# Kernel tuning notes

Hardware: AMD Instinct MI355X
Metric: run time of the kernel (lower is better)

Reference implementation:

```python
import jax, jax.numpy as jnp
import numpy as np

B, S, T = 32, 128, 64
V, E, H = 32000, 256, 512


def setup_inputs() -> dict:
    key = jax.random.key(0)
    ks = jax.random.split(key, 32)
    n = jax.random.normal

    def lin(k, fi, fo):
        kw, kb = jax.random.split(k)
        s = 1.0 / np.sqrt(fi)
        return (jax.random.uniform(kw, (fi, fo), jnp.float32, -s, s),
                jax.random.uniform(kb, (fo,), jnp.float32, -s, s))

    W_enc, b_enc = lin(ks[4], 2 * H, H)      # attention.enc_h_in
    W_prev, b_prev = lin(ks[5], H, H)        # attention.prev_s_in
    W_att, b_att = lin(ks[6], H, 1)          # attention.linear
    Wi_g, bi_g = lin(ks[7], E, 2 * H)        # cell.input_weights
    Wh_g, bh_g = lin(ks[8], H, 2 * H)        # cell.hidden_weights
    Wc_g, bc_g = lin(ks[9], 2 * H, 2 * H)    # cell.ctx_weights
    Wi, bi = lin(ks[10], E, H)               # cell.input_in
    Wh, bh = lin(ks[11], H, H)               # cell.hidden_in
    Wc, bc = lin(ks[12], 2 * H, H)           # cell.ctx_in
    W_out, b_out = lin(ks[13], H, V)         # dec2word

    return dict(
        content=n(ks[0], (B, H), jnp.float32),
        sentiment=n(ks[1], (B, H), jnp.float32),
        hiddens=n(ks[2], (B, S, 2 * H), jnp.float32),
        target=jax.random.randint(ks[3], (B, T), 0, V, jnp.int32),
        embed=n(ks[14], (V, E), jnp.float32) * 0.02,
        W_enc=W_enc, b_enc=b_enc, W_prev=W_prev, b_prev=b_prev,
        W_att=W_att, b_att=b_att,
        Wi_g=Wi_g, bi_g=bi_g, Wh_g=Wh_g, bh_g=bh_g, Wc_g=Wc_g, bc_g=bc_g,
        Wi=Wi, bi=bi, Wh=Wh, bh=bh, Wc=Wc, bc=bc,
        W_out=W_out, b_out=b_out,
    )


def reference(content, sentiment, hiddens, target, embed,
              W_enc, b_enc, W_prev, b_prev, W_att, b_att,
              Wi_g, bi_g, Wh_g, bh_g, Wc_g, bc_g,
              Wi, bi, Wh, bh, Wc, bc, W_out, b_out):
    tgt_emb = embed[target]                       # [B, T, E]
    enc_proj = hiddens @ W_enc + b_enc            # [B, S, H], timestep-invariant

    def step(prev_s, x_t):
        # additive attention
        q = prev_s @ W_prev + b_prev              # [B, H]
        h = jnp.tanh(enc_proj + q[:, None, :])    # [B, S, H]
        score = h @ W_att + b_att                 # [B, S, 1]
        alpha = jax.nn.softmax(score, axis=1)     # over source positions
        ctx = jnp.einsum('bsi,bsh->bh', alpha, hiddens)  # [B, 2H]
        # GRU-like cell (original uses only the first gate, as written)
        gates = x_t @ Wi_g + bi_g + prev_s @ Wh_g + bh_g + ctx @ Wc_g + bc_g
        reset_gate, _update_gate = jnp.split(gates, 2, axis=1)
        r = jax.nn.sigmoid(reset_gate)
        s_tilde = jnp.tanh(x_t @ Wi + bi + prev_s @ Wh + bh + ctx @ Wc + bc)
        new_s = (1.0 - r) * prev_s + r * s_tilde
        return new_s, new_s

    _, dec_h = jax.lax.scan(step, content, jnp.swapaxes(tgt_emb, 0, 1))
    dec_h = jnp.swapaxes(dec_h, 0, 1)             # [B, T, H]
    style_logits = sentiment @ W_out + b_out      # [B, V], same every step
    outputs = (dec_h @ W_out + b_out) + 0.5 * style_logits[:, None, :]
    return outputs                                # [B, T, V]
```

## Files before the change

### kernel.cpp

```cpp
#include <hip/hip_runtime.h>
#include <hip/hip_bf16.h>
#include <math.h>

#define NB 32
#define NS 128
#define NT 64
#define NV 32000
#define NE 256
#define NH 512

typedef short s16x8 __attribute__((ext_vector_type(8)));
typedef float f32x4 __attribute__((ext_vector_type(4)));

__device__ __forceinline__ unsigned short f2bf(float x) {
    union { float f; unsigned u; } v; v.f = x;
    unsigned r = v.u + 0x7FFFu + ((v.u >> 16) & 1u);
    return (unsigned short)(r >> 16);
}
__device__ __forceinline__ float bf2f(short h) {
    union { unsigned u; float f; } x;
    x.u = ((unsigned)(unsigned short)h) << 16;
    return x.f;
}

__device__ __forceinline__ void bar_lgkm() {
    asm volatile("s_waitcnt lgkmcnt(0)" ::: "memory");
    __builtin_amdgcn_sched_barrier(0);
    __builtin_amdgcn_s_barrier();
    __builtin_amdgcn_sched_barrier(0);
}

__device__ __forceinline__ void st_pt(unsigned long long* p, unsigned pay, unsigned tag) {
    unsigned long long v = (unsigned long long)pay | ((unsigned long long)tag << 32);
    asm volatile("global_store_dwordx2 %0, %1, off sc0 sc1" :: "v"(p), "v"(v) : "memory");
}
__device__ __forceinline__ void ld8_pt(const unsigned long long* b0, unsigned long long* v) {
    unsigned long long v0, v1, v2, v3, v4, v5, v6, v7;
    asm volatile(
        "global_load_dwordx2 %0, %8, off sc0 sc1\n\t"
        "global_load_dwordx2 %1, %9, off sc0 sc1\n\t"
        "global_load_dwordx2 %2, %10, off sc0 sc1\n\t"
        "global_load_dwordx2 %3, %11, off sc0 sc1\n\t"
        "global_load_dwordx2 %4, %12, off sc0 sc1\n\t"
        "global_load_dwordx2 %5, %13, off sc0 sc1\n\t"
        "global_load_dwordx2 %6, %14, off sc0 sc1\n\t"
        "global_load_dwordx2 %7, %15, off sc0 sc1\n\t"
        "s_waitcnt vmcnt(0)"
        : "=&v"(v0), "=&v"(v1), "=&v"(v2), "=&v"(v3),
          "=&v"(v4), "=&v"(v5), "=&v"(v6), "=&v"(v7)
        : "v"(b0), "v"(b0 + 1024), "v"(b0 + 2048), "v"(b0 + 3072),
          "v"(b0 + 4096), "v"(b0 + 5120), "v"(b0 + 6144), "v"(b0 + 7168)
        : "memory");
    v[0] = v0; v[1] = v1; v[2] = v2; v[3] = v3;
    v[4] = v4; v[5] = v5; v[6] = v6; v[7] = v7;
}
__device__ __forceinline__ void ld3_pt(const unsigned long long* p0,
                                       const unsigned long long* p1,
                                       const unsigned long long* p2,
                                       unsigned long long& a, unsigned long long& b,
                                       unsigned long long& c) {
    asm volatile(
        "global_load_dwordx2 %0, %3, off sc0 sc1\n\t"
        "global_load_dwordx2 %1, %4, off sc0 sc1\n\t"
        "global_load_dwordx2 %2, %5, off sc0 sc1\n\t"
        "s_waitcnt vmcnt(0)"
        : "=&v"(a), "=&v"(b), "=&v"(c)
        : "v"(p0), "v"(p1), "v"(p2)
        : "memory");
}

__global__ void build_wfrag_k(const float* __restrict__ Wp,
                              const float* __restrict__ Whg,
                              const float* __restrict__ Wh,
                              unsigned short* __restrict__ wfrag) {
    int blk = blockIdx.x;
    int lane = threadIdx.x;
    int ct = blk >> 4, kt = blk & 15;
    int c = ct * 16 + (lane & 15);
    int kb = kt * 32 + (lane >> 4) * 8;
    s16x8 v;
#pragma unroll
    for (int j = 0; j < 8; ++j) {
        int k = kb + j;
        float x;
        if (c < 512)       x = Wp[k * 512 + c];
        else if (c < 1024) x = Whg[k * 1024 + (c - 512)];
        else               x = Wh[k * 512 + (c - 1024)];
        v[j] = (short)f2bf(x);
    }
    ((s16x8*)wfrag)[blk * 64 + lane] = v;
}

template<int MODE>
__global__ __launch_bounds__(256, 2) void gemm_mfma(
    const float* __restrict__ Af, const unsigned short* __restrict__ Abf,
    const int* __restrict__ gidx,
    const float* __restrict__ B0, const float* __restrict__ B1, const float* __restrict__ B2,
    const float* __restrict__ e0, const float* __restrict__ e1, const float* __restrict__ e2,
    const float* __restrict__ e3, const float* __restrict__ e4, const float* __restrict__ e5,
    void* __restrict__ O0v, void* __restrict__ O1v, void* __restrict__ O2v)
{
    constexpr int M   = (MODE == 0) ? 4096 : 2048;
    constexpr int K   = (MODE == 0) ? 1024 : ((MODE == 1) ? 256 : 512);
    constexpr int LDA = (MODE == 0) ? 1024 : ((MODE == 1) ? 256 : 512);
    constexpr int MB  = M / 128;

    const int bm = blockIdx.x % MB, bn = blockIdx.x / MB;
    const int m0 = bm * 128, n0 = bn * 128;

    const float* Bp; int ldb, coff;
    if constexpr (MODE == 0) {
        int sub = n0 >> 9;
        Bp   = (sub == 0) ? B0 : (sub == 1) ? B1 : B2;
        ldb  = (sub == 1) ? 1024 : 512;
        coff = n0 & 511;
    } else if constexpr (MODE == 1) {
        if (n0 < 512) { Bp = B0; ldb = 1024; coff = n0; }
        else          { Bp = B1; ldb = 512;  coff = n0 - 512; }
    } else {
        Bp = B0; ldb = 32000; coff = n0;
    }

    __shared__ unsigned short As[128 * 40];
    __shared__ unsigned short Bs[128 * 40];

    const int tid = threadIdx.x, lane = tid & 63, w = tid >> 6;
    const int wr = w >> 1, wc = w & 1;
    const int k0f = (lane >> 4) * 8;
    const int rsel = lane & 15;

    f32x4 acc[4][4];
#pragma unroll
    for (int i = 0; i < 4; ++i)
#pragma unroll
        for (int j = 0; j < 4; ++j) { f32x4 z = {0.f, 0.f, 0.f, 0.f}; acc[i][j] = z; }

    for (int kt = 0; kt < K / 32; ++kt) {
        const int k0 = kt * 32;
        __syncthreads();
#pragma unroll
        for (int i = 0; i < 16; ++i) {
            int idx = tid + i * 256;
            int r = idx >> 5, k = idx & 31;
            unsigned short v;
            if constexpr (MODE == 2) {
                v = Abf[(size_t)(m0 + r) * LDA + k0 + k];
            } else if constexpr (MODE == 1) {
                int g = gidx[m0 + r];
                v = f2bf(Af[(size_t)g * 256 + k0 + k]);
            } else {
                v = f2bf(Af[(size_t)(m0 + r) * LDA + k0 + k]);
            }
            As[r * 40 + k] = v;
        }
#pragma unroll
        for (int i = 0; i < 16; ++i) {
            int idx = tid + i * 256;
            int k = idx >> 7, c = idx & 127;
            Bs[c * 40 + k] = f2bf(Bp[(size_t)(k0 + k) * ldb + coff + c]);
        }
        __syncthreads();

        s16x8 af[4], bf[4];
#pragma unroll
        for (int i = 0; i < 4; ++i)
            af[i] = *(const s16x8*)&As[(wr * 64 + i * 16 + rsel) * 40 + k0f];
#pragma unroll
        for (int j = 0; j < 4; ++j)
            bf[j] = *(const s16x8*)&Bs[(wc * 64 + j * 16 + rsel) * 40 + k0f];
#pragma unroll
        for (int i = 0; i < 4; ++i)
#pragma unroll
            for (int j = 0; j < 4; ++j)
                acc[i][j] = __builtin_amdgcn_mfma_f32_16x16x32_bf16(af[i], bf[j], acc[i][j], 0, 0, 0);
    }

    const int rg = (lane >> 4) * 4;
#pragma unroll
    for (int i = 0; i < 4; ++i)
#pragma unroll
        for (int j = 0; j < 4; ++j) {
            int row0 = m0 + wr * 64 + i * 16 + rg;
            int col  = n0 + wc * 64 + j * 16 + rsel;
            if constexpr (MODE == 0) {
                int sub = col >> 9;
                if (sub == 0) {
                    unsigned short* Ta = (unsigned short*)O0v;
#pragma unroll
                    for (int r = 0; r < 4; ++r)
                        Ta[(size_t)(row0 + r) * 512 + col] = f2bf(tanhf(acc[i][j][r] + e0[col]));
                } else {
                    int h = col & 511;
                    int bb = row0 >> 7, s0 = row0 & 127;
                    unsigned long long pk = 0;
#pragma unroll
                    for (int r = 0; r < 4; ++r)
                        pk |= (unsigned long long)f2bf(acc[i][j][r]) << (16 * r);
                    unsigned short* dstp = (sub == 1) ? (unsigned short*)O1v : (unsigned short*)O2v;
                    *(unsigned long long*)&dstp[(size_t)((bb * 512 + h) * 128 + s0)] = pk;
                }
            } else if constexpr (MODE == 1) {
                float* Of = (float*)O0v;
                float bias;
                if (col < 512) bias = e0[col] + e1[col] + e2[col];
                else { int h = col - 512; bias = e3[h] + e4[h] + e5[h]; }
#pragma unroll
                for (int r = 0; r < 4; ++r)
                    Of[(size_t)(row0 + r) * 1024 + col] = acc[i][j][r] + bias;
            } else {
                float* Of = (float*)O0v;
#pragma unroll
                for (int r = 0; r < 4; ++r)
                    Of[(size_t)(row0 + r) * 32000 + col] = acc[i][j][r] + 1.5f * e0[col];
            }
        }
}

__global__ __launch_bounds__(1024) void scan_df(
    const float* __restrict__ content, const float* __restrict__ sentiment,
    const float* __restrict__ b_prev,  const float* __restrict__ W_att,
    const unsigned short* __restrict__ Ta_bf,
    const unsigned short* __restrict__ hWcg_t,
    const unsigned short* __restrict__ hWc_t,
    const float* __restrict__ xgxs, const unsigned short* __restrict__ wfrag,
    unsigned long long* __restrict__ Spl, unsigned long long* __restrict__ Upl,
    unsigned short* __restrict__ dh)
{
    const int b = blockIdx.x;
    const int tid = threadIdx.x, lane = tid & 63, w = tid >> 6;

    __shared__ unsigned short W_lds[3 * 16 * 64 * 8];
    __shared__ unsigned short S_lds[32 * 536];
    __shared__ float tq[512];
    __shared__ float sc[128], al[128];
    __shared__ float cg[512], cs[512];

    {
        const s16x8* src = (const s16x8*)wfrag + (size_t)b * (3 * 16 * 64);
        s16x8* dst = (s16x8*)W_lds;
        for (int i = tid; i < 3 * 16 * 64; i += 1024) dst[i] = src[i];
    }
    float s_reg = 0.f, senth = 0.f, bprev_h = 0.f;
    if (tid < 512) {
        s_reg   = content[b * 512 + tid];
        senth   = 0.5f * sentiment[b * 512 + tid];
        bprev_h = b_prev[tid];
    }
    float wv[8];
    {
        const f32x4* wa = (const f32x4*)&W_att[lane * 8];
        f32x4 a0 = wa[0], a1 = wa[1];
#pragma unroll
        for (int j = 0; j < 4; ++j) { wv[j] = a0[j]; wv[4 + j] = a1[j]; }
    }
    const int kbase = (lane >> 4) * 8;
    const int mat = tid >> 9, hh = tid & 511;
    const s16x8* Mp = (const s16x8*)((mat ? hWc_t : hWcg_t) + ((size_t)(b * 512 + hh)) * 128);

    if (tid < 512) {
        float nsn = __shfl_down(s_reg, 1, 64);
        if (!(lane & 1)) {
            unsigned pay = (unsigned)f2bf(s_reg) | ((unsigned)f2bf(nsn) << 16);
            st_pt(&Spl[b * 256 + (tid >> 1)], pay, 1u);
        }
    }

    for (int t = 0; t < 64; ++t) {
        const unsigned want = (unsigned)(t + 1);
        const size_t xrow = (size_t)b * 64 + t;
        float xg_pre = 0.f, xs_pre = 0.f;
        if (tid < 512) {
            xg_pre = xgxs[xrow * 1024 + tid];
            xs_pre = xgxs[xrow * 1024 + 512 + tid];
        }

        {
            unsigned long long v[8];
            const unsigned long long* base = &Spl[tid];
            ld8_pt(base, v);
            for (;;) {
                bool ok = true;
#pragma unroll
                for (int ii = 0; ii < 8; ++ii) ok &= ((unsigned)(v[ii] >> 32) == want);
                if (ok) break;
                __builtin_amdgcn_s_sleep(1);
                ld8_pt(base, v);
            }
#pragma unroll
            for (int ii = 0; ii < 8; ++ii) {
                int idx = tid + ii * 1024;
                int r = idx >> 8, c = (idx & 255) * 2;
                *(unsigned*)&S_lds[r * 536 + c] = (unsigned)v[ii];
            }
        }
        bar_lgkm();

        if (w < 6) {
            const int mt = w & 1, ct = w >> 1;
            const int arow = mt * 16 + (lane & 15);
            f32x4 ae = {0.f, 0.f, 0.f, 0.f}, ao = {0.f, 0.f, 0.f, 0.f};
            const s16x8* wl = (const s16x8*)W_lds;
#pragma unroll
            for (int kt = 0; kt < 16; kt += 2) {
                s16x8 a0 = *(const s16x8*)&S_lds[arow * 536 + kt * 32 + kbase];
                s16x8 a1 = *(const s16x8*)&S_lds[arow * 536 + (kt + 1) * 32 + kbase];
                ae = __builtin_amdgcn_mfma_f32_16x16x32_bf16(a0, wl[(ct * 16 + kt) * 64 + lane], ae, 0, 0, 0);
                ao = __builtin_amdgcn_mfma_f32_16x16x32_bf16(a1, wl[(ct * 16 + kt + 1) * 64 + lane], ao, 0, 0, 0);
            }
            f32x4 a4 = ae + ao;
            const int cout = b * 48 + ct * 16 + (lane & 15);
            const int rbase = mt * 16 + (lane >> 4) * 4;
#pragma unroll
            for (int r = 0; r < 4; ++r)
                st_pt(&Upl[(size_t)(rbase + r) * 1536 + cout], __float_as_uint(a4[r]), want);
        }

        float guv = 0.f, suv = 0.f;
        if (tid < 512) {
            unsigned long long u0, u1, u2;
            const unsigned long long* q0 = &Upl[b * 1536 + tid];
            const unsigned long long* q1 = &Upl[b * 1536 + 512 + tid];
            const unsigned long long* q2 = &Upl[b * 1536 + 1024 + tid];
            ld3_pt(q0, q1, q2, u0, u1, u2);
            while (((unsigned)(u0 >> 32) != want) | ((unsigned)(u1 >> 32) != want) |
                   ((unsigned)(u2 >> 32) != want)) {
                __builtin_amdgcn_s_sleep(1);
                ld3_pt(q0, q1, q2, u0, u1, u2);
            }
            float qv = __uint_as_float((unsigned)u0);
            guv = __uint_as_float((unsigned)u1);
            suv = __uint_as_float((unsigned)u2);
            tq[tid] = tanhf(qv + bprev_h);
        }
        bar_lgkm();

        {
            float tqv[8];
            const f32x4* tp = (const f32x4*)&tq[lane * 8];
            f32x4 t0 = tp[0], t1 = tp[1];
#pragma unroll
            for (int j = 0; j < 4; ++j) { tqv[j] = t0[j]; tqv[4 + j] = t1[j]; }
#pragma unroll
            for (int s8 = 0; s8 < 8; ++s8) {
                int s = w * 8 + s8;
                s16x8 tv = *(const s16x8*)&Ta_bf[((size_t)(b * 128 + s)) * 512 + lane * 8];
                float a = 0.f;
#pragma unroll
                for (int j = 0; j < 8; ++j) {
                    float ta = bf2f(tv[j]);
                    float num = ta + tqv[j];
                    float den = fmaf(ta, tqv[j], 1.0f);
                    a = fmaf(wv[j], num * __builtin_amdgcn_rcpf(den), a);
                }
#pragma unroll
                for (int off = 32; off; off >>= 1) a += __shfl_xor(a, off, 64);
                if (lane == 0) sc[s] = a;
            }
        }

        s16x8 hw[8];
#pragma unroll
        for (int q = 0; q < 8; ++q) hw[q] = Mp[q];

        bar_lgkm();
        if (w == 0) {
            float v0 = sc[lane], v1 = sc[lane + 64];
            float m = fmaxf(v0, v1);
#pragma unroll
            for (int off = 32; off; off >>= 1) m = fmaxf(m, __shfl_xor(m, off, 64));
            float p0 = __expf(v0 - m), p1 = __expf(v1 - m);
            float sm = p0 + p1;
#pragma unroll
            for (int off = 32; off; off >>= 1) sm += __shfl_xor(sm, off, 64);
            float inv = __builtin_amdgcn_rcpf(sm);
            al[lane] = p0 * inv; al[lane + 64] = p1 * inv;
        }
        bar_lgkm();

        {
            float a0 = 0.f, a1 = 0.f;
#pragma unroll
            for (int q = 0; q < 8; ++q) {
                s16x8 v = hw[q];
#pragma unroll
                for (int j = 0; j < 8; j += 2) {
                    a0 = fmaf(al[q * 8 + j],     bf2f(v[j]),     a0);
                    a1 = fmaf(al[q * 8 + j + 1], bf2f(v[j + 1]), a1);
                }
            }
#pragma unroll
            for (int q = 8; q < 16; ++q) {
                s16x8 v = Mp[q];
#pragma unroll
                for (int j = 0; j < 8; j += 2) {
                    a0 = fmaf(al[q * 8 + j],     bf2f(v[j]),     a0);
                    a1 = fmaf(al[q * 8 + j + 1], bf2f(v[j + 1]), a1);
                }
            }
            if (mat) cs[hh] = a0 + a1; else cg[hh] = a0 + a1;
        }
        bar_lgkm();

        if (tid < 512) {
            int h = tid;
            float g  = guv + xg_pre + cg[h];
            float r  = __builtin_amdgcn_rcpf(1.0f + __expf(-g));
            float sp = suv + xs_pre + cs[h];
            float e  = __expf(2.0f * sp);
            float st = 1.0f - 2.0f * __builtin_amdgcn_rcpf(e + 1.0f);
            float ns = s_reg + r * (st - s_reg);
            s_reg = ns;
            dh[xrow * 512 + h] = f2bf(ns + senth);
            if (t < 63) {
                float nsn = __shfl_down(ns, 1, 64);
                if (!(lane & 1)) {
                    unsigned pay = (unsigned)f2bf(ns) | ((unsigned)f2bf(nsn) << 16);
                    st_pt(&Spl[b * 256 + (h >> 1)], pay, (unsigned)(t + 2));
                }
            }
        }
        bar_lgkm();
    }
}

extern "C" void kernel_launch(void* const* d_in, const int* in_sizes, int n_in,
                              void* d_out, int out_size, void* d_ws, size_t ws_size,
                              hipStream_t stream) {
    const float* content  = (const float*)d_in[0];
    const float* sentiment= (const float*)d_in[1];
    const float* hiddens  = (const float*)d_in[2];
    const int*   target   = (const int*)  d_in[3];
    const float* embed    = (const float*)d_in[4];
    const float* W_enc = (const float*)d_in[5];  const float* b_enc = (const float*)d_in[6];
    const float* W_prev= (const float*)d_in[7];  const float* b_prev= (const float*)d_in[8];
    const float* W_att = (const float*)d_in[9];
    const float* Wi_g  = (const float*)d_in[11]; const float* bi_g  = (const float*)d_in[12];
    const float* Wh_g  = (const float*)d_in[13]; const float* bh_g  = (const float*)d_in[14];
    const float* Wc_g  = (const float*)d_in[15]; const float* bc_g  = (const float*)d_in[16];
    const float* Wi    = (const float*)d_in[17]; const float* bi    = (const float*)d_in[18];
    const float* Wh    = (const float*)d_in[19]; const float* bh    = (const float*)d_in[20];
    const float* Wc    = (const float*)d_in[21]; const float* bc    = (const float*)d_in[22];
    const float* W_out = (const float*)d_in[23]; const float* b_out = (const float*)d_in[24];
    float* out = (float*)d_out;

    char* ws = (char*)d_ws;
    unsigned short* wfrag = (unsigned short*)ws;
    unsigned long long* Spl = (unsigned long long*)(ws + 0x180000);
    unsigned long long* Upl = (unsigned long long*)(ws + 0x190000);
    unsigned short* Ta_bf   = (unsigned short*)(ws + 0x200000);
    unsigned short* hWcg_t  = (unsigned short*)(ws + 0x600000);
    unsigned short* hWc_t   = (unsigned short*)(ws + 0xA00000);
    float* xgxs     = (float*)(ws + 0xE00000);
    unsigned short* dh      = (unsigned short*)(ws + 0x1600000);

    hipMemsetAsync(ws + 0x180000, 0, 0x70000, stream);

    build_wfrag_k<<<96 * 16, 64, 0, stream>>>(W_prev, Wh_g, Wh, wfrag);

    gemm_mfma<0><<<32 * 12, 256, 0, stream>>>(
        hiddens, nullptr, nullptr, W_enc, Wc_g, Wc,
        b_enc, nullptr, nullptr, nullptr, nullptr, nullptr,
        (void*)Ta_bf, (void*)hWcg_t, (void*)hWc_t);

    gemm_mfma<1><<<16 * 8, 256, 0, stream>>>(
        embed, nullptr, target, Wi_g, Wi, nullptr,
        bi_g, bh_g, bc_g, bi, bh, bc,
        (void*)xgxs, nullptr, nullptr);

    scan_df<<<NB, 1024, 0, stream>>>(
        content, sentiment, b_prev, W_att, Ta_bf, hWcg_t, hWc_t,
        xgxs, wfrag, Spl, Upl, dh);

    gemm_mfma<2><<<16 * 250, 256, 0, stream>>>(
        nullptr, dh, nullptr, W_out, nullptr, nullptr,
        b_out, nullptr, nullptr, nullptr, nullptr, nullptr,
        (void*)out, nullptr, nullptr);

    (void)in_sizes; (void)n_in; (void)out_size; (void)ws_size;
}
```

Baseline: 1.359 ms.

## Fuse output projection into scan kernel, overlapping vocab GEMM with recurrence

Merges the sequential scan and the vocabulary projection GEMM into one persistent launch. Thirty-two blocks run the recurrence and publish per-batch progress counters every 8 timesteps. The remaining 224 blocks spin on those counters and compute 256x256 output tiles for finished timestep groups, so the large GEMM overlaps the latency-bound scan. In exchange the output GEMM now loads its tiles through coherent, uncached loads and converts W_out to bf16 on the fly. The extra co-resident blocks may also compete with the scan blocks for compute units, and the design relies on all blocks being resident at once to avoid deadlock.

```diff
diff --git a/kernel.cpp b/kernel.cpp
--- a/kernel.cpp
+++ b/kernel.cpp
@@ -11,6 +11,7 @@
 
 typedef short s16x8 __attribute__((ext_vector_type(8)));
 typedef float f32x4 __attribute__((ext_vector_type(4)));
+typedef unsigned u32x4 __attribute__((ext_vector_type(4)));
 
 __device__ __forceinline__ unsigned short f2bf(float x) {
     union { float f; unsigned u; } v; v.f = x;
@@ -33,6 +34,21 @@
 __device__ __forceinline__ void st_pt(unsigned long long* p, unsigned pay, unsigned tag) {
     unsigned long long v = (unsigned long long)pay | ((unsigned long long)tag << 32);
     asm volatile("global_store_dwordx2 %0, %1, off sc0 sc1" :: "v"(p), "v"(v) : "memory");
+}
+__device__ __forceinline__ void st_coh32(unsigned* p, unsigned v) {
+    asm volatile("global_store_dword %0, %1, off sc0 sc1" :: "v"(p), "v"(v) : "memory");
+}
+__device__ __forceinline__ unsigned ld_coh32(const unsigned* p) {
+    unsigned v;
+    asm volatile("global_load_dword %0, %1, off sc0 sc1\n\ts_waitcnt vmcnt(0)"
+                 : "=v"(v) : "v"(p) : "memory");
+    return v;
+}
+__device__ __forceinline__ u32x4 ld_coh_x4(const void* p) {
+    u32x4 v;
+    asm volatile("global_load_dwordx4 %0, %1, off sc0 sc1\n\ts_waitcnt vmcnt(0)"
+                 : "=&v"(v) : "v"(p) : "memory");
+    return v;
 }
 __device__ __forceinline__ void ld8_pt(const unsigned long long* b0, unsigned long long* v) {
     unsigned long long v0, v1, v2, v3, v4, v5, v6, v7;
@@ -101,8 +117,8 @@
     void* __restrict__ O0v, void* __restrict__ O1v, void* __restrict__ O2v)
 {
     constexpr int M   = (MODE == 0) ? 4096 : 2048;
-    constexpr int K   = (MODE == 0) ? 1024 : ((MODE == 1) ? 256 : 512);
-    constexpr int LDA = (MODE == 0) ? 1024 : ((MODE == 1) ? 256 : 512);
+    constexpr int K   = (MODE == 0) ? 1024 : 256;
+    constexpr int LDA = (MODE == 0) ? 1024 : 256;
     constexpr int MB  = M / 128;
 
     const int bm = blockIdx.x % MB, bn = blockIdx.x / MB;
@@ -114,11 +130,9 @@
         Bp   = (sub == 0) ? B0 : (sub == 1) ? B1 : B2;
         ldb  = (sub == 1) ? 1024 : 512;
         coff = n0 & 511;
-    } else if constexpr (MODE == 1) {
+    } else {
         if (n0 < 512) { Bp = B0; ldb = 1024; coff = n0; }
         else          { Bp = B1; ldb = 512;  coff = n0 - 512; }
-    } else {
-        Bp = B0; ldb = 32000; coff = n0;
     }
 
     __shared__ unsigned short As[128 * 40];
@@ -143,9 +157,7 @@
             int idx = tid + i * 256;
             int r = idx >> 5, k = idx & 31;
             unsigned short v;
-            if constexpr (MODE == 2) {
-                v = Abf[(size_t)(m0 + r) * LDA + k0 + k];
-            } else if constexpr (MODE == 1) {
+            if constexpr (MODE == 1) {
                 int g = gidx[m0 + r];
                 v = f2bf(Af[(size_t)g * 256 + k0 + k]);
             } else {
@@ -199,7 +211,7 @@
                     unsigned short* dstp = (sub == 1) ? (unsigned short*)O1v : (unsigned short*)O2v;
                     *(unsigned long long*)&dstp[(size_t)((bb * 512 + h) * 128 + s0)] = pk;
                 }
-            } else if constexpr (MODE == 1) {
+            } else {
                 float* Of = (float*)O0v;
                 float bias;
                 if (col < 512) bias = e0[col] + e1[col] + e2[col];
@@ -207,16 +219,11 @@
 #pragma unroll
                 for (int r = 0; r < 4; ++r)
                     Of[(size_t)(row0 + r) * 1024 + col] = acc[i][j][r] + bias;
-            } else {
-                float* Of = (float*)O0v;
-#pragma unroll
-                for (int r = 0; r < 4; ++r)
-                    Of[(size_t)(row0 + r) * 32000 + col] = acc[i][j][r] + 1.5f * e0[col];
-            }
-        }
-}
-
-__global__ __launch_bounds__(1024) void scan_df(
+            }
+        }
+}
+
+__global__ __launch_bounds__(1024) void fused_scan_out(
     const float* __restrict__ content, const float* __restrict__ sentiment,
     const float* __restrict__ b_prev,  const float* __restrict__ W_att,
     const unsigned short* __restrict__ Ta_bf,
@@ -224,202 +231,274 @@
     const unsigned short* __restrict__ hWc_t,
     const float* __restrict__ xgxs, const unsigned short* __restrict__ wfrag,
     unsigned long long* __restrict__ Spl, unsigned long long* __restrict__ Upl,
-    unsigned short* __restrict__ dh)
+    unsigned short* __restrict__ dh, unsigned* __restrict__ prog,
+    const float* __restrict__ W_out, const float* __restrict__ b_out,
+    float* __restrict__ out)
 {
-    const int b = blockIdx.x;
+    __shared__ __attribute__((aligned(16))) char smem[90624];
     const int tid = threadIdx.x, lane = tid & 63, w = tid >> 6;
 
-    __shared__ unsigned short W_lds[3 * 16 * 64 * 8];
-    __shared__ unsigned short S_lds[32 * 536];
-    __shared__ float tq[512];
-    __shared__ float sc[128], al[128];
-    __shared__ float cg[512], cs[512];
-
-    {
-        const s16x8* src = (const s16x8*)wfrag + (size_t)b * (3 * 16 * 64);
-        s16x8* dst = (s16x8*)W_lds;
-        for (int i = tid; i < 3 * 16 * 64; i += 1024) dst[i] = src[i];
-    }
-    float s_reg = 0.f, senth = 0.f, bprev_h = 0.f;
-    if (tid < 512) {
-        s_reg   = content[b * 512 + tid];
-        senth   = 0.5f * sentiment[b * 512 + tid];
-        bprev_h = b_prev[tid];
-    }
-    float wv[8];
-    {
-        const f32x4* wa = (const f32x4*)&W_att[lane * 8];
-        f32x4 a0 = wa[0], a1 = wa[1];
-#pragma unroll
-        for (int j = 0; j < 4; ++j) { wv[j] = a0[j]; wv[4 + j] = a1[j]; }
-    }
-    const int kbase = (lane >> 4) * 8;
-    const int mat = tid >> 9, hh = tid & 511;
-    const s16x8* Mp = (const s16x8*)((mat ? hWc_t : hWcg_t) + ((size_t)(b * 512 + hh)) * 128);
-
-    if (tid < 512) {
-        float nsn = __shfl_down(s_reg, 1, 64);
-        if (!(lane & 1)) {
-            unsigned pay = (unsigned)f2bf(s_reg) | ((unsigned)f2bf(nsn) << 16);
-            st_pt(&Spl[b * 256 + (tid >> 1)], pay, 1u);
-        }
-    }
-
-    for (int t = 0; t < 64; ++t) {
-        const unsigned want = (unsigned)(t + 1);
-        const size_t xrow = (size_t)b * 64 + t;
-        float xg_pre = 0.f, xs_pre = 0.f;
+    if (blockIdx.x < NB) {
+        const int b = blockIdx.x;
+        unsigned short* W_lds = (unsigned short*)smem;
+        unsigned short* S_lds = (unsigned short*)(smem + 49152);
+        float* tq = (float*)(smem + 83456);
+        float* sc = (float*)(smem + 85504);
+        float* al = (float*)(smem + 86016);
+        float* cg = (float*)(smem + 86528);
+        float* cs = (float*)(smem + 88576);
+
+        {
+            const s16x8* src = (const s16x8*)wfrag + (size_t)b * (3 * 16 * 64);
+            s16x8* dst = (s16x8*)W_lds;
+            for (int i = tid; i < 3 * 16 * 64; i += 1024) dst[i] = src[i];
+        }
+        float s_reg = 0.f, senth = 0.f, bprev_h = 0.f;
         if (tid < 512) {
-            xg_pre = xgxs[xrow * 1024 + tid];
-            xs_pre = xgxs[xrow * 1024 + 512 + tid];
-        }
-
+            s_reg   = content[b * 512 + tid];
+            senth   = 0.5f * sentiment[b * 512 + tid];
+            bprev_h = b_prev[tid];
+        }
+        float wv[8];
         {
-            unsigned long long v[8];
-            const unsigned long long* base = &Spl[tid];
-            ld8_pt(base, v);
-            for (;;) {
-                bool ok = true;
-#pragma unroll
-                for (int ii = 0; ii < 8; ++ii) ok &= ((unsigned)(v[ii] >> 32) == want);
-                if (ok) break;
-                __builtin_amdgcn_s_sleep(1);
+            const f32x4* wa = (const f32x4*)&W_att[lane * 8];
+            f32x4 a0 = wa[0], a1 = wa[1];
+#pragma unroll
+            for (int j = 0; j < 4; ++j) { wv[j] = a0[j]; wv[4 + j] = a1[j]; }
+        }
+        const int kbase = (lane >> 4) * 8;
+        const int mat = tid >> 9, hh = tid & 511;
+        const s16x8* Mp = (const s16x8*)((mat ? hWc_t : hWcg_t) + ((size_t)(b * 512 + hh)) * 128);
+
+        if (tid < 512) {
+            float nsn = __shfl_down(s_reg, 1, 64);
+            if (!(lane & 1)) {
+                unsigned pay = (unsigned)f2bf(s_reg) | ((unsigned)f2bf(nsn) << 16);
+                st_pt(&Spl[b * 256 + (tid >> 1)], pay, 1u);
+            }
+        }
+
+        for (int t = 0; t < 64; ++t) {
+            const unsigned want = (unsigned)(t + 1);
+            float xg_pre = 0.f, xs_pre = 0.f;
+            if (tid < 512) {
+                xg_pre = xgxs[((size_t)b * 64 + t) * 1024 + tid];
+                xs_pre = xgxs[((size_t)b * 64 + t) * 1024 + 512 + tid];
+            }
+
+            {
+                unsigned long long v[8];
+                const unsigned long long* base = &Spl[tid];
                 ld8_pt(base, v);
-            }
-#pragma unroll
-            for (int ii = 0; ii < 8; ++ii) {
-                int idx = tid + ii * 1024;
-                int r = idx >> 8, c = (idx & 255) * 2;
-                *(unsigned*)&S_lds[r * 536 + c] = (unsigned)v[ii];
-            }
-        }
-        bar_lgkm();
-
-        if (w < 6) {
-            const int mt = w & 1, ct = w >> 1;
-            const int arow = mt * 16 + (lane & 15);
-            f32x4 ae = {0.f, 0.f, 0.f, 0.f}, ao = {0.f, 0.f, 0.f, 0.f};
-            const s16x8* wl = (const s16x8*)W_lds;
-#pragma unroll
-            for (int kt = 0; kt < 16; kt += 2) {
-                s16x8 a0 = *(const s16x8*)&S_lds[arow * 536 + kt * 32 + kbase];
-                s16x8 a1 = *(const s16x8*)&S_lds[arow * 536 + (kt + 1) * 32 + kbase];
-                ae = __builtin_amdgcn_mfma_f32_16x16x32_bf16(a0, wl[(ct * 16 + kt) * 64 + lane], ae, 0, 0, 0);
-                ao = __builtin_amdgcn_mfma_f32_16x16x32_bf16(a1, wl[(ct * 16 + kt + 1) * 64 + lane], ao, 0, 0, 0);
-            }
-            f32x4 a4 = ae + ao;
-            const int cout = b * 48 + ct * 16 + (lane & 15);
-            const int rbase = mt * 16 + (lane >> 4) * 4;
-#pragma unroll
-            for (int r = 0; r < 4; ++r)
-                st_pt(&Upl[(size_t)(rbase + r) * 1536 + cout], __float_as_uint(a4[r]), want);
-        }
-
-        float guv = 0.f, suv = 0.f;
-        if (tid < 512) {
-            unsigned long long u0, u1, u2;
-            const unsigned long long* q0 = &Upl[b * 1536 + tid];
-            const unsigned long long* q1 = &Upl[b * 1536 + 512 + tid];
-            const unsigned long long* q2 = &Upl[b * 1536 + 1024 + tid];
-            ld3_pt(q0, q1, q2, u0, u1, u2);
-            while (((unsigned)(u0 >> 32) != want) | ((unsigned)(u1 >> 32) != want) |
-                   ((unsigned)(u2 >> 32) != want)) {
-                __builtin_amdgcn_s_sleep(1);
+                for (;;) {
+                    bool ok = true;
+#pragma unroll
+                    for (int ii = 0; ii < 8; ++ii) ok &= ((unsigned)(v[ii] >> 32) == want);
+                    if (ok) break;
+                    __builtin_amdgcn_s_sleep(1);
+                    ld8_pt(base, v);
+                }
+#pragma unroll
+                for (int ii = 0; ii < 8; ++ii) {
+                    int idx = tid + ii * 1024;
+                    int r = idx >> 8, c = (idx & 255) * 2;
+                    *(unsigned*)&S_lds[r * 536 + c] = (unsigned)v[ii];
+                }
+            }
+            bar_lgkm();
+
+            if (w < 6) {
+                const int mt = w & 1, ct = w >> 1;
+                const int arow = mt * 16 + (lane & 15);
+                f32x4 ae = {0.f, 0.f, 0.f, 0.f}, ao = {0.f, 0.f, 0.f, 0.f};
+                const s16x8* wl = (const s16x8*)W_lds;
+#pragma unroll
+                for (int kt = 0; kt < 16; kt += 2) {
+                    s16x8 a0 = *(const s16x8*)&S_lds[arow * 536 + kt * 32 + kbase];
+                    s16x8 a1 = *(const s16x8*)&S_lds[arow * 536 + (kt + 1) * 32 + kbase];
+                    ae = __builtin_amdgcn_mfma_f32_16x16x32_bf16(a0, wl[(ct * 16 + kt) * 64 + lane], ae, 0, 0, 0);
+                    ao = __builtin_amdgcn_mfma_f32_16x16x32_bf16(a1, wl[(ct * 16 + kt + 1) * 64 + lane], ao, 0, 0, 0);
+                }
+                f32x4 a4 = ae + ao;
+                const int cout = b * 48 + ct * 16 + (lane & 15);
+                const int rbase = mt * 16 + (lane >> 4) * 4;
+#pragma unroll
+                for (int r = 0; r < 4; ++r)
+                    st_pt(&Upl[(size_t)(rbase + r) * 1536 + cout], __float_as_uint(a4[r]), want);
+            }
+
+            float guv = 0.f, suv = 0.f;
+            if (tid < 512) {
+                unsigned long long u0, u1, u2;
+                const unsigned long long* q0 = &Upl[b * 1536 + tid];
+                const unsigned long long* q1 = &Upl[b * 1536 + 512 + tid];
+                const unsigned long long* q2 = &Upl[b * 1536 + 1024 + tid];
                 ld3_pt(q0, q1, q2, u0, u1, u2);
-            }
-            float qv = __uint_as_float((unsigned)u0);
-            guv = __uint_as_float((unsigned)u1);
-            suv = __uint_as_float((unsigned)u2);
-            tq[tid] = tanhf(qv + bprev_h);
-        }
-        bar_lgkm();
-
-        {
-            float tqv[8];
-            const f32x4* tp = (const f32x4*)&tq[lane * 8];
-            f32x4 t0 = tp[0], t1 = tp[1];
-#pragma unroll
-            for (int j = 0; j < 4; ++j) { tqv[j] = t0[j]; tqv[4 + j] = t1[j]; }
-#pragma unroll
-            for (int s8 = 0; s8 < 8; ++s8) {
-                int s = w * 8 + s8;
-                s16x8 tv = *(const s16x8*)&Ta_bf[((size_t)(b * 128 + s)) * 512 + lane * 8];
-                float a = 0.f;
-#pragma unroll
-                for (int j = 0; j < 8; ++j) {
-                    float ta = bf2f(tv[j]);
-                    float num = ta + tqv[j];
-                    float den = fmaf(ta, tqv[j], 1.0f);
-                    a = fmaf(wv[j], num * __builtin_amdgcn_rcpf(den), a);
-                }
-#pragma unroll
-                for (int off = 32; off; off >>= 1) a += __shfl_xor(a, off, 64);
-                if (lane == 0) sc[s] = a;
-            }
-        }
-
-        s16x8 hw[8];
-#pragma unroll
-        for (int q = 0; q < 8; ++q) hw[q] = Mp[q];
-
-        bar_lgkm();
-        if (w == 0) {
-            float v0 = sc[lane], v1 = sc[lane + 64];
-            float m = fmaxf(v0, v1);
-#pragma unroll
-            for (int off = 32; off; off >>= 1) m = fmaxf(m, __shfl_xor(m, off, 64));
-            float p0 = __expf(v0 - m), p1 = __expf(v1 - m);
-            float sm = p0 + p1;
-#pragma unroll
-            for (int off = 32; off; off >>= 1) sm += __shfl_xor(sm, off, 64);
-            float inv = __builtin_amdgcn_rcpf(sm);
-            al[lane] = p0 * inv; al[lane + 64] = p1 * inv;
-        }
-        bar_lgkm();
-
-        {
-            float a0 = 0.f, a1 = 0.f;
-#pragma unroll
-            for (int q = 0; q < 8; ++q) {
-                s16x8 v = hw[q];
-#pragma unroll
-                for (int j = 0; j < 8; j += 2) {
-                    a0 = fmaf(al[q * 8 + j],     bf2f(v[j]),     a0);
-                    a1 = fmaf(al[q * 8 + j + 1], bf2f(v[j + 1]), a1);
-                }
-            }
-#pragma unroll
-            for (int q = 8; q < 16; ++q) {
-                s16x8 v = Mp[q];
-#pragma unroll
-                for (int j = 0; j < 8; j += 2) {
-                    a0 = fmaf(al[q * 8 + j],     bf2f(v[j]),     a0);
-                    a1 = fmaf(al[q * 8 + j + 1], bf2f(v[j + 1]), a1);
-                }
-            }
-            if (mat) cs[hh] = a0 + a1; else cg[hh] = a0 + a1;
-        }
-        bar_lgkm();
-
-        if (tid < 512) {
-            int h = tid;
-            float g  = guv + xg_pre + cg[h];
-            float r  = __builtin_amdgcn_rcpf(1.0f + __expf(-g));
-            float sp = suv + xs_pre + cs[h];
-            float e  = __expf(2.0f * sp);
-            float st = 1.0f - 2.0f * __builtin_amdgcn_rcpf(e + 1.0f);
-            float ns = s_reg + r * (st - s_reg);
-            s_reg = ns;
-            dh[xrow * 512 + h] = f2bf(ns + senth);
-            if (t < 63) {
-                float nsn = __shfl_down(ns, 1, 64);
+                while (((unsigned)(u0 >> 32) != want) | ((unsigned)(u1 >> 32) != want) |
+                       ((unsigned)(u2 >> 32) != want)) {
+                    __builtin_amdgcn_s_sleep(1);
+                    ld3_pt(q0, q1, q2, u0, u1, u2);
+                }
+                float qv = __uint_as_float((unsigned)u0);
+                guv = __uint_as_float((unsigned)u1);
+                suv = __uint_as_float((unsigned)u2);
+                tq[tid] = tanhf(qv + bprev_h);
+            }
+            bar_lgkm();
+
+            {
+                float tqv[8];
+                const f32x4* tp = (const f32x4*)&tq[lane * 8];
+                f32x4 t0 = tp[0], t1 = tp[1];
+#pragma unroll
+                for (int j = 0; j < 4; ++j) { tqv[j] = t0[j]; tqv[4 + j] = t1[j]; }
+#pragma unroll
+                for (int s8 = 0; s8 < 8; ++s8) {
+                    int s = w * 8 + s8;
+                    s16x8 tv = *(const s16x8*)&Ta_bf[((size_t)(b * 128 + s)) * 512 + lane * 8];
+                    float a = 0.f;
+#pragma unroll
+                    for (int j = 0; j < 8; ++j) {
+                        float ta = bf2f(tv[j]);
+                        float num = ta + tqv[j];
+                        float den = fmaf(ta, tqv[j], 1.0f);
+                        a = fmaf(wv[j], num * __builtin_amdgcn_rcpf(den), a);
+                    }
+#pragma unroll
+                    for (int off = 32; off; off >>= 1) a += __shfl_xor(a, off, 64);
+                    if (lane == 0) sc[s] = a;
+                }
+            }
+            bar_lgkm();
+            if (w == 0) {
+                float v0 = sc[lane], v1 = sc[lane + 64];
+                float m = fmaxf(v0, v1);
+#pragma unroll
+                for (int off = 32; off; off >>= 1) m = fmaxf(m, __shfl_xor(m, off, 64));
+                float p0 = __expf(v0 - m), p1 = __expf(v1 - m);
+                float sm = p0 + p1;
+#pragma unroll
+                for (int off = 32; off; off >>= 1) sm += __shfl_xor(sm, off, 64);
+                float inv = __builtin_amdgcn_rcpf(sm);
+                al[lane] = p0 * inv; al[lane + 64] = p1 * inv;
+            }
+            bar_lgkm();
+            {
+                float a0 = 0.f, a1 = 0.f;
+#pragma unroll
+                for (int q = 0; q < 16; ++q) {
+                    s16x8 v = Mp[q];
+#pragma unroll
+                    for (int j = 0; j < 8; j += 2) {
+                        a0 = fmaf(al[q * 8 + j],     bf2f(v[j]),     a0);
+                        a1 = fmaf(al[q * 8 + j + 1], bf2f(v[j + 1]), a1);
+                    }
+                }
+                if (mat) cs[hh] = a0 + a1; else cg[hh] = a0 + a1;
+            }
+            bar_lgkm();
+            if (tid < 512) {
+                int h = tid;
+                float g  = guv + xg_pre + cg[h];
+                float r  = __builtin_amdgcn_rcpf(1.0f + __expf(-g));
+                float sp = suv + xs_pre + cs[h];
+                float e  = __expf(2.0f * sp);
+                float st = 1.0f - 2.0f * __builtin_amdgcn_rcpf(e + 1.0f);
+                float ns = s_reg + r * (st - s_reg);
+                s_reg = ns;
+                float dv = ns + senth;
+                float dvn = __shfl_down(dv, 1, 64);
                 if (!(lane & 1)) {
-                    unsigned pay = (unsigned)f2bf(ns) | ((unsigned)f2bf(nsn) << 16);
-                    st_pt(&Spl[b * 256 + (h >> 1)], pay, (unsigned)(t + 2));
-                }
-            }
-        }
-        bar_lgkm();
+                    unsigned pk = (unsigned)f2bf(dv) | ((unsigned)f2bf(dvn) << 16);
+                    st_coh32((unsigned*)dh + ((((size_t)t * 32 + b) * 512 + h) >> 1), pk);
+                }
+                if (t < 63) {
+                    float nsn = __shfl_down(ns, 1, 64);
+                    if (!(lane & 1)) {
+                        unsigned pay = (unsigned)f2bf(ns) | ((unsigned)f2bf(nsn) << 16);
+                        st_pt(&Spl[b * 256 + (h >> 1)], pay, (unsigned)(t + 2));
+                    }
+                }
+            }
+            if ((t & 7) == 7) asm volatile("s_waitcnt vmcnt(0)" ::: "memory");
+            bar_lgkm();
+            if ((t & 7) == 7 && tid == 0)
+                st_coh32(&prog[b * 16], (unsigned)(t + 1));
+        }
+    } else {
+        unsigned short* As = (unsigned short*)smem;
+        unsigned short* Bs = (unsigned short*)(smem + 20480);
+        const int k4 = blockIdx.x - NB;
+        const int wr = w >> 2, wc = w & 3;
+        const int k0f = (lane >> 4) * 8;
+        const int rsel = lane & 15;
+        const int rg = (lane >> 4) * 4;
+        const int ar = tid >> 2, akofs = (tid & 3) * 8;
+        const int bk = tid >> 5, bc8 = (tid & 31) * 8;
+
+        for (int idx = k4; idx < 1000; idx += 224) {
+            const int tm = idx / 125, tn = idx - tm * 125;
+            const unsigned need = (unsigned)(tm * 8 + 8);
+            if (w == 0) {
+                for (;;) {
+                    unsigned v = 0xFFFFFFFFu;
+                    if (lane < 32) v = ld_coh32(&prog[lane * 16]);
+                    if (__all(v >= need)) break;
+                    __builtin_amdgcn_s_sleep(32);
+                }
+            }
+            __syncthreads();
+
+            const int m0 = tm * 256, n0 = tn * 256;
+            f32x4 acc[4][4];
+#pragma unroll
+            for (int i = 0; i < 4; ++i)
+#pragma unroll
+                for (int j = 0; j < 4; ++j) { f32x4 z = {0.f, 0.f, 0.f, 0.f}; acc[i][j] = z; }
+
+            for (int kt = 0; kt < 16; ++kt) {
+                const int k0 = kt * 32;
+                __syncthreads();
+                {
+                    u32x4 a = ld_coh_x4(&dh[(size_t)(m0 + ar) * 512 + k0 + akofs]);
+                    *(u32x4*)&As[ar * 40 + akofs] = a;
+                }
+                {
+                    const float* bp = &W_out[(size_t)(k0 + bk) * 32000 + n0 + bc8];
+#pragma unroll
+                    for (int j = 0; j < 8; ++j) Bs[(bc8 + j) * 40 + bk] = f2bf(bp[j]);
+                }
+                __syncthreads();
+
+                s16x8 af[4], bfr[4];
+#pragma unroll
+                for (int i = 0; i < 4; ++i)
+                    af[i] = *(const s16x8*)&As[(wr * 64 + i * 16 + rsel) * 40 + k0f];
+#pragma unroll
+                for (int j = 0; j < 4; ++j)
+                    bfr[j] = *(const s16x8*)&Bs[(wc * 64 + j * 16 + rsel) * 40 + k0f];
+#pragma unroll
+                for (int i = 0; i < 4; ++i)
+#pragma unroll
+                    for (int j = 0; j < 4; ++j)
+                        acc[i][j] = __builtin_amdgcn_mfma_f32_16x16x32_bf16(af[i], bfr[j], acc[i][j], 0, 0, 0);
+            }
+
+#pragma unroll
+            for (int i = 0; i < 4; ++i)
+#pragma unroll
+                for (int j = 0; j < 4; ++j) {
+                    int trow0 = m0 + wr * 64 + i * 16 + rg;
+                    int col   = n0 + wc * 64 + j * 16 + rsel;
+                    float bb_ = 1.5f * b_out[col];
+#pragma unroll
+                    for (int r = 0; r < 4; ++r) {
+                        int trow = trow0 + r;
+                        int bb = trow & 31, tt = trow >> 5;
+                        out[(size_t)(bb * 64 + tt) * 32000 + col] = acc[i][j][r] + bb_;
+                    }
+                }
+        }
     }
 }
 
@@ -447,13 +526,14 @@
     unsigned short* wfrag = (unsigned short*)ws;
     unsigned long long* Spl = (unsigned long long*)(ws + 0x180000);
     unsigned long long* Upl = (unsigned long long*)(ws + 0x190000);
+    unsigned* prog = (unsigned*)(ws + 0x1F0000);
     unsigned short* Ta_bf   = (unsigned short*)(ws + 0x200000);
     unsigned short* hWcg_t  = (unsigned short*)(ws + 0x600000);
     unsigned short* hWc_t   = (unsigned short*)(ws + 0xA00000);
     float* xgxs     = (float*)(ws + 0xE00000);
     unsigned short* dh      = (unsigned short*)(ws + 0x1600000);
 
-    hipMemsetAsync(ws + 0x180000, 0, 0x70000, stream);
+    hipMemsetAsync(ws + 0x180000, 0, 0x70800, stream);
 
     build_wfrag_k<<<96 * 16, 64, 0, stream>>>(W_prev, Wh_g, Wh, wfrag);
 
@@ -467,14 +547,9 @@
         bi_g, bh_g, bc_g, bi, bh, bc,
         (void*)xgxs, nullptr, nullptr);
 
-    scan_df<<<NB, 1024, 0, stream>>>(
+    fused_scan_out<<<256, 1024, 0, stream>>>(
         content, sentiment, b_prev, W_att, Ta_bf, hWcg_t, hWc_t,
-        xgxs, wfrag, Spl, Upl, dh);
-
-    gemm_mfma<2><<<16 * 250, 256, 0, stream>>>(
-        nullptr, dh, nullptr, W_out, nullptr, nullptr,
-        b_out, nullptr, nullptr, nullptr, nullptr, nullptr,
-        (void*)out, nullptr, nullptr);
+        xgxs, wfrag, Spl, Upl, dh, prog, W_out, b_out, out);
 
     (void)in_sizes; (void)n_in; (void)out_size; (void)ws_size;
 }
```

New measurement: 1.337 ms. No clear change (-1.6%).
